# Performance work log

Measured on AMD Instinct MI355X. Metric: run time of the kernel, lower is better.

The kernel has to match this reference:

```python
import jax, jax.numpy as jnp
import numpy as np

N_NODES = 100000
N_EDGES = 3200000
D_IN = 128
D_HID = 128
N_CLASSES = 40


def setup_inputs() -> dict:
    key = jax.random.key(0)
    ks = jax.random.split(key, 8)
    x = jax.random.normal(ks[0], (N_NODES, D_IN), dtype=jnp.float32)
    edge_index = jax.random.randint(ks[1], (2, N_EDGES), 0, N_NODES, dtype=jnp.int64)
    s1 = 1.0 / np.sqrt(D_IN)
    s2 = 1.0 / np.sqrt(D_HID)
    W1 = jax.random.normal(ks[2], (D_IN, D_HID), dtype=jnp.float32) * s1
    b1 = jnp.zeros((D_HID,), dtype=jnp.float32)
    W2 = jax.random.normal(ks[3], (D_HID, D_HID), dtype=jnp.float32) * s2
    b2 = jnp.zeros((D_HID,), dtype=jnp.float32)
    Wl = jax.random.normal(ks[4], (D_HID, N_CLASSES), dtype=jnp.float32) * s2
    bl = jnp.zeros((N_CLASSES,), dtype=jnp.float32)
    return {"x": x, "edge_index": edge_index, "W1": W1, "b1": b1,
            "W2": W2, "b2": b2, "Wl": Wl, "bl": bl}


def _gcn_conv(x, W, b, src, dst, inv_sqrt_deg, n_nodes):
    # h = X @ W  (linear transform first: cheaper when out_dim <= in_dim)
    h = x @ W  # [N, d_out]
    # symmetric normalization: norm_e = deg(src)^-1/2 * deg(dst)^-1/2
    norm = inv_sqrt_deg[src] * inv_sqrt_deg[dst]  # [E]
    msg = h[src] * norm[:, None]                  # gather + scale  [E, d_out]
    out = jax.ops.segment_sum(msg, dst, num_segments=n_nodes)  # scatter-add
    return out + b


def reference(x, edge_index, W1, b1, W2, b2, Wl, bl):
    n = x.shape[0]
    # GCNConv adds self-loops before normalization (PyG default)
    loops = jnp.arange(n, dtype=edge_index.dtype)
    src = jnp.concatenate([edge_index[0], loops])
    dst = jnp.concatenate([edge_index[1], loops])
    deg = jax.ops.segment_sum(jnp.ones_like(dst, dtype=x.dtype), dst, num_segments=n)
    inv_sqrt_deg = jnp.where(deg > 0, jax.lax.rsqrt(deg), 0.0)

    h = _gcn_conv(x, W1, b1, src, dst, inv_sqrt_deg, n)
    h = jax.nn.relu(h)
    h = _gcn_conv(h, W2, b2, src, dst, inv_sqrt_deg, n)
    h = jax.nn.relu(h)
    return h @ Wl + bl
```

## Files before the change

kernel.cpp:

```cpp
#include <hip/hip_runtime.h>
#include <hip/hip_bf16.h>

typedef _Float16 f16;
typedef _Float16 f16x8 __attribute__((ext_vector_type(8)));

#define D 128
#define N_CLS 40
#define BN 128
#define NBMAX 1024


__global__ __launch_bounds__(256) void k_hist(const int* __restrict__ dst,
                                              int* __restrict__ bcnt, int e) {
  __shared__ int lh[NBMAX];
  for (int j = threadIdx.x; j < NBMAX; j += 256) lh[j] = 0;
  __syncthreads();
  int stride = gridDim.x * blockDim.x;
  for (int q = blockIdx.x * blockDim.x + threadIdx.x; q < e; q += stride)
    atomicAdd(&lh[dst[q] >> 7], 1);
  __syncthreads();
  for (int j = threadIdx.x; j < NBMAX; j += 256)
    if (lh[j]) atomicAdd(&bcnt[j], lh[j]);
}

__global__ __launch_bounds__(1024) void k_bscan(const int* __restrict__ bcnt,
                                                int* __restrict__ bbase,
                                                int* __restrict__ bcur) {
  __shared__ int sums[NBMAX];
  int t = threadIdx.x;
  int c = bcnt[t];
  sums[t] = c;
  __syncthreads();
  for (int off = 1; off < NBMAX; off <<= 1) {
    int a = (t >= off) ? sums[t - off] : 0;
    __syncthreads();
    sums[t] += a;
    __syncthreads();
  }
  bbase[t] = sums[t] - c;
  bcur[t] = sums[t] - c;
}

__global__ __launch_bounds__(256) void k_place(const int* __restrict__ src,
                                               const int* __restrict__ dst,
                                               int* __restrict__ bcur,
                                               unsigned int* __restrict__ binned,
                                               int e, int nwg) {
  __shared__ int lh[NBMAX];
  __shared__ int lofs[NBMAX];
  __shared__ int lcur[NBMAX];
  int chunk = (e + nwg - 1) / nwg;
  int lo = blockIdx.x * chunk;
  int hi = min(e, lo + chunk);
  int t = threadIdx.x;
  for (int j = t; j < NBMAX; j += 256) { lh[j] = 0; lcur[j] = 0; }
  __syncthreads();
  for (int q = lo + t; q < hi; q += 256) atomicAdd(&lh[dst[q] >> 7], 1);
  __syncthreads();
  for (int j = t; j < NBMAX; j += 256) {
    int c = lh[j];
    lofs[j] = c ? atomicAdd(&bcur[j], c) : 0;
  }
  __syncthreads();
  for (int q = lo + t; q < hi; q += 256) {
    int d = dst[q];
    int b = d >> 7;
    int r = atomicAdd(&lcur[b], 1);
    binned[lofs[b] + r] = ((unsigned int)(d & 127) << 17) | (unsigned int)src[q];
  }
}

__global__ __launch_bounds__(256) void k_csr(const unsigned int* __restrict__ binned,
                                             const int* __restrict__ bbase,
                                             int* __restrict__ csr,
                                             int* __restrict__ deg,
                                             float* __restrict__ isd,
                                             int* __restrict__ row_start, int n) {
  int b = blockIdx.x;
  int lo = bbase[b], hi = bbase[b + 1];
  __shared__ int h[BN];
  __shared__ int sc[BN];
  __shared__ int cur[BN];
  int t = threadIdx.x;
  if (t < BN) h[t] = 0;
  __syncthreads();
  for (int q = lo + t; q < hi; q += 256) atomicAdd(&h[binned[q] >> 17], 1);
  __syncthreads();
  if (t < BN) sc[t] = h[t];
  __syncthreads();
  for (int off = 1; off < BN; off <<= 1) {
    int a = 0;
    if (t < BN && t >= off) a = sc[t - off];
    __syncthreads();
    if (t < BN) sc[t] += a;
    __syncthreads();
  }
  if (t < BN) {
    int excl = sc[t] - h[t];
    cur[t] = lo + excl;
    int i = b * BN + t;
    if (i < n) {
      deg[i] = h[t];
      isd[i] = rsqrtf((float)(h[t] + 1));
      row_start[i] = lo + excl;
    }
  }
  __syncthreads();
  for (int q = lo + t; q < hi; q += 256) {
    unsigned int u = binned[q];
    int p = atomicAdd(&cur[u >> 17], 1);
    csr[p] = (int)(u & 0x1FFFF);
  }
}

template <bool HALF_IN>
__global__ __launch_bounds__(256) void k_gemm_t(const void* __restrict__ Xv,
                                                const float* __restrict__ W,
                                                const float* __restrict__ isd,
                                                f16* __restrict__ HS, int n) {
  __shared__ float Xt[64][D + 4];
  __shared__ float Wb[32][D + 4];
  const size_t ss = (size_t)n * 16;
  int t = threadIdx.x;
  int r0 = blockIdx.x * 64;
  if (!HALF_IN) {
    const float* X = (const float*)Xv;
    for (int q = t; q < 64 * 32; q += 256) {
      int row = q >> 5, cb = (q & 31) << 2;
      float4 v = {0.f, 0.f, 0.f, 0.f};
      if (r0 + row < n) v = *(const float4*)(X + (size_t)(r0 + row) * D + cb);
      *(float4*)&Xt[row][cb] = v;
    }
  } else {
    const f16* X = (const f16*)Xv;
    for (int q = t; q < 64 * 16; q += 256) {
      int row = q >> 4, cb = (q & 15) << 3;
      f16x8 v = 0;
      if (r0 + row < n)
        v = *(const f16x8*)(X + (size_t)(cb >> 4) * ss +
                            (size_t)(r0 + row) * 16 + (cb & 15));
      float* xp = &Xt[row][cb];
#pragma unroll
      for (int j = 0; j < 8; ++j) xp[j] = (float)v[j];
    }
  }
  int tr = ((t >> 4) & 15) << 2;
  int tc = (t & 15) << 3;
  float acc[4][8];
#pragma unroll
  for (int i = 0; i < 4; ++i)
#pragma unroll
    for (int j = 0; j < 8; ++j) acc[i][j] = 0.f;

  for (int hh = 0; hh < 4; ++hh) {
    __syncthreads();
    for (int q = t; q < 32 * 32; q += 256) {
      int row = q >> 5, cb = (q & 31) << 2;
      *(float4*)&Wb[row][cb] = *(const float4*)(W + (size_t)(hh * 32 + row) * D + cb);
    }
    __syncthreads();
#pragma unroll 4
    for (int k = 0; k < 32; ++k) {
      float4 u0 = *(const float4*)&Wb[k][tc];
      float4 u1 = *(const float4*)&Wb[k][tc + 4];
      float bv[8] = {u0.x, u0.y, u0.z, u0.w, u1.x, u1.y, u1.z, u1.w};
      int kk = hh * 32 + k;
#pragma unroll
      for (int i = 0; i < 4; ++i) {
        float a = Xt[tr + i][kk];
#pragma unroll
        for (int j = 0; j < 8; ++j) acc[i][j] += a * bv[j];
      }
    }
  }
#pragma unroll
  for (int i = 0; i < 4; ++i) {
    int row = r0 + tr + i;
    if (row < n) {
      float s = isd[row];
      f16x8 ov;
#pragma unroll
      for (int j = 0; j < 8; ++j) ov[j] = (f16)(s * acc[i][j]);
      *(f16x8*)(HS + (size_t)(tc >> 4) * ss + (size_t)row * 16 + (tc & 15)) = ov;
    }
  }
}

__device__ inline f16x8 shfl_xor_f16x8(f16x8 v, int m) {
  union { f16x8 h; int i[4]; } u;
  u.h = v;
#pragma unroll
  for (int k = 0; k < 4; ++k) u.i[k] = __shfl_xor(u.i[k], m);
  return u.h;
}

__global__ __launch_bounds__(256) void k_aggs(const f16* __restrict__ HS,
                                              const int* __restrict__ csr,
                                              const int* __restrict__ row_start,
                                              const int* __restrict__ deg,
                                              const float* __restrict__ isd,
                                              const float* __restrict__ bias,
                                              f16* __restrict__ G, int n) {
  const size_t ss = (size_t)n * 16;
  int t = threadIdx.x;
  int wave = t >> 6, lane = t & 63;
  int g = lane >> 4, r = lane & 15;
  int s = blockIdx.x & 7;
  int i0 = ((blockIdx.x >> 3) << 4) + (wave << 2) + g;
  bool ok = i0 < n;
  int i = ok ? i0 : n - 1;
  int hf = r & 1, er = r >> 1;
  int dg = deg[i];
  const int* cp = csr + row_start[i];
  const f16* sb = HS + (size_t)s * ss + (size_t)hf * 8;
  f16x8 a0 = (f16x8)0, a1 = (f16x8)0;
  if (dg > 0) {
    int dgm = dg - 1;
    int iA = cp[min(er, dgm)];
    int iB = cp[min(er + 8, dgm)];
    for (int u = 0; u < dg; u += 16) {
      int cA = iA, cB = iB;
      iA = cp[min(u + 16 + er, dgm)];
      iB = cp[min(u + 24 + er, dgm)];
      if (u + er < dg)
        a0 += *(const f16x8*)(sb + ((size_t)(unsigned)cA << 4));
      if (u + 8 + er < dg)
        a1 += *(const f16x8*)(sb + ((size_t)(unsigned)cB << 4));
    }
  }
  f16x8 tv = a0 + a1;
  tv += shfl_xor_f16x8(tv, 2);
  tv += shfl_xor_f16x8(tv, 4);
  tv += shfl_xor_f16x8(tv, 8);
  f16x8 sv = *(const f16x8*)(HS + (size_t)s * ss + (size_t)i * 16 + hf * 8);
  float di = isd[i];
  const float* bp = bias + s * 16 + hf * 8;
  float4 b0 = *(const float4*)bp;
  float4 b1 = *(const float4*)(bp + 4);
  float bv[8] = {b0.x, b0.y, b0.z, b0.w, b1.x, b1.y, b1.z, b1.w};
  f16x8 ov;
#pragma unroll
  for (int j = 0; j < 8; ++j) {
    float v = di * ((float)tv[j] + (float)sv[j]) + bv[j];
    v = v > 0.f ? v : 0.f;
    ov[j] = (f16)v;
  }
  if (ok && r < 2)
    *(f16x8*)(G + (size_t)s * ss + (size_t)i * 16 + hf * 8) = ov;
}

__global__ __launch_bounds__(256) void k_cls(const f16* __restrict__ H,
                                             const float* __restrict__ Wl,
                                             const float* __restrict__ bl,
                                             float* __restrict__ out, int n) {
  const size_t ss = (size_t)n * 16;
  int wv = threadIdx.x >> 6;
  int ir = (blockIdx.x << 2) + wv;
  int i = ir < n ? ir : n - 1;
  int lane = threadIdx.x & 63;
  __shared__ float tt[4][D];
  if (lane < 16) {
    int s = lane >> 1, hf = lane & 1;
    f16x8 v = *(const f16x8*)(H + (size_t)s * ss + (size_t)i * 16 + hf * 8);
    float* dp = &tt[wv][s * 16 + hf * 8];
#pragma unroll
    for (int j = 0; j < 8; ++j) dp[j] = (float)v[j];
  }
  __syncthreads();
  if (ir < n && lane < N_CLS) {
    float o = bl[lane];
#pragma unroll 4
    for (int k = 0; k < D; k += 4) {
      float4 t4 = *(const float4*)&tt[wv][k];
      o += t4.x * Wl[(k + 0) * N_CLS + lane];
      o += t4.y * Wl[(k + 1) * N_CLS + lane];
      o += t4.z * Wl[(k + 2) * N_CLS + lane];
      o += t4.w * Wl[(k + 3) * N_CLS + lane];
    }
    out[(size_t)ir * N_CLS + lane] = o;
  }
}

extern "C" void kernel_launch(void* const* d_in, const int* in_sizes, int n_in,
                              void* d_out, int out_size, void* d_ws, size_t ws_size,
                              hipStream_t stream) {
  const float* x  = (const float*)d_in[0];
  const int*   ei = (const int*)d_in[1];
  const float* W1 = (const float*)d_in[2];
  const float* b1 = (const float*)d_in[3];
  const float* W2 = (const float*)d_in[4];
  const float* b2 = (const float*)d_in[5];
  const float* Wl = (const float*)d_in[6];
  const float* bl = (const float*)d_in[7];
  float* out = (float*)d_out;

  const int n = in_sizes[0] / D;
  const int e = in_sizes[1] / 2;
  const int* src = ei;
  const int* dst = ei + e;
  const int nb = (n + BN - 1) / BN;

  char* ws = (char*)d_ws;
  size_t off = 0;
  auto alloc = [&](size_t bytes) -> void* {
    void* p = ws + off;
    off += (bytes + 255) & ~(size_t)255;
    return p;
  };
  int*   bcnt      = (int*)alloc(NBMAX * 4);
  int*   bbase     = (int*)alloc(NBMAX * 4);
  int*   bcur      = (int*)alloc(NBMAX * 4);
  int*   deg       = (int*)alloc((size_t)n * 4);
  int*   row_start = (int*)alloc((size_t)n * 4);
  float* isd       = (float*)alloc((size_t)n * 4);
  int*   csr       = (int*)alloc((size_t)e * 4);
  f16*   hA        = (f16*)alloc((size_t)n * D * 2);
  f16*   hB        = (f16*)alloc((size_t)n * D * 2);
  unsigned int* binned = (unsigned int*)hA;

  hipMemsetAsync(bcnt, 0, NBMAX * 4, stream);

  const int nwg_place = 512;
  k_hist<<<1024, 256, 0, stream>>>(dst, bcnt, e);
  k_bscan<<<1, 1024, 0, stream>>>(bcnt, bbase, bcur);
  k_place<<<nwg_place, 256, 0, stream>>>(src, dst, bcur, binned, e, nwg_place);
  k_csr<<<nb, 256, 0, stream>>>(binned, bbase, csr, deg, isd, row_start, n);

  int gblocks = (n + 63) / 64;
  int ablocks = ((n + 15) / 16) * 8;
  k_gemm_t<false><<<gblocks, 256, 0, stream>>>(x, W1, isd, hA, n);
  k_aggs<<<ablocks, 256, 0, stream>>>(hA, csr, row_start, deg, isd, b1, hB, n);
  k_gemm_t<true><<<gblocks, 256, 0, stream>>>(hB, W2, isd, hA, n);
  k_aggs<<<ablocks, 256, 0, stream>>>(hA, csr, row_start, deg, isd, b2, hB, n);
  k_cls<<<(n + 3) / 4, 256, 0, stream>>>(hB, Wl, bl, out, n);
}
```

Before: 679.9 us.

## Use row-major aggregation output, widen edge unroll, batch classifier rows per block

The aggregation kernel now writes its output row-major ([n, 128] f16) instead of in 16-column slabs. The half-precision GEMM input path and the classifier read that layout with contiguous row loads. The edge loop keeps four accumulators and prefetches 32 neighbor indices per iteration instead of 16, to expose more memory-level parallelism on the gathers. The classifier stages 16 rows per block in shared memory, with each wave computing 4 rows. The padded D+1 row stride makes the float4 shared-memory reads misaligned for odd rows, which risks slower LDS access or incorrect behaviour.

```diff
diff --git a/kernel.cpp b/kernel.cpp
--- a/kernel.cpp
+++ b/kernel.cpp
@@ -136,9 +136,7 @@
     for (int q = t; q < 64 * 16; q += 256) {
       int row = q >> 4, cb = (q & 15) << 3;
       f16x8 v = 0;
-      if (r0 + row < n)
-        v = *(const f16x8*)(X + (size_t)(cb >> 4) * ss +
-                            (size_t)(r0 + row) * 16 + (cb & 15));
+      if (r0 + row < n) v = *(const f16x8*)(X + (size_t)(r0 + row) * D + cb);
       float* xp = &Xt[row][cb];
 #pragma unroll
       for (int j = 0; j < 8; ++j) xp[j] = (float)v[j];
@@ -212,29 +210,37 @@
   int hf = r & 1, er = r >> 1;
   int dg = deg[i];
   const int* cp = csr + row_start[i];
-  const f16* sb = HS + (size_t)s * ss + (size_t)hf * 8;
-  f16x8 a0 = (f16x8)0, a1 = (f16x8)0;
+  const f16* sb = HS + (size_t)s * ss + (size_t)(hf << 3);
+  f16x8 a0 = (f16x8)0, a1 = (f16x8)0, a2 = (f16x8)0, a3 = (f16x8)0;
   if (dg > 0) {
     int dgm = dg - 1;
     int iA = cp[min(er, dgm)];
     int iB = cp[min(er + 8, dgm)];
-    for (int u = 0; u < dg; u += 16) {
-      int cA = iA, cB = iB;
-      iA = cp[min(u + 16 + er, dgm)];
-      iB = cp[min(u + 24 + er, dgm)];
+    int iC = cp[min(er + 16, dgm)];
+    int iD = cp[min(er + 24, dgm)];
+    for (int u = 0; u < dg; u += 32) {
+      int cA = iA, cB = iB, cC = iC, cD = iD;
+      iA = cp[min(u + 32 + er, dgm)];
+      iB = cp[min(u + 40 + er, dgm)];
+      iC = cp[min(u + 48 + er, dgm)];
+      iD = cp[min(u + 56 + er, dgm)];
       if (u + er < dg)
         a0 += *(const f16x8*)(sb + ((size_t)(unsigned)cA << 4));
       if (u + 8 + er < dg)
         a1 += *(const f16x8*)(sb + ((size_t)(unsigned)cB << 4));
-    }
-  }
-  f16x8 tv = a0 + a1;
+      if (u + 16 + er < dg)
+        a2 += *(const f16x8*)(sb + ((size_t)(unsigned)cC << 4));
+      if (u + 24 + er < dg)
+        a3 += *(const f16x8*)(sb + ((size_t)(unsigned)cD << 4));
+    }
+  }
+  f16x8 tv = (a0 + a1) + (a2 + a3);
   tv += shfl_xor_f16x8(tv, 2);
   tv += shfl_xor_f16x8(tv, 4);
   tv += shfl_xor_f16x8(tv, 8);
-  f16x8 sv = *(const f16x8*)(HS + (size_t)s * ss + (size_t)i * 16 + hf * 8);
+  f16x8 sv = *(const f16x8*)(HS + (size_t)s * ss + (size_t)i * 16 + (hf << 3));
   float di = isd[i];
-  const float* bp = bias + s * 16 + hf * 8;
+  const float* bp = bias + s * 16 + (hf << 3);
   float4 b0 = *(const float4*)bp;
   float4 b1 = *(const float4*)(bp + 4);
   float bv[8] = {b0.x, b0.y, b0.z, b0.w, b1.x, b1.y, b1.z, b1.w};
@@ -246,38 +252,43 @@
     ov[j] = (f16)v;
   }
   if (ok && r < 2)
-    *(f16x8*)(G + (size_t)s * ss + (size_t)i * 16 + hf * 8) = ov;
+    *(f16x8*)(G + (size_t)i * D + s * 16 + (hf << 3)) = ov;
 }
 
 __global__ __launch_bounds__(256) void k_cls(const f16* __restrict__ H,
                                              const float* __restrict__ Wl,
                                              const float* __restrict__ bl,
                                              float* __restrict__ out, int n) {
-  const size_t ss = (size_t)n * 16;
-  int wv = threadIdx.x >> 6;
-  int ir = (blockIdx.x << 2) + wv;
-  int i = ir < n ? ir : n - 1;
-  int lane = threadIdx.x & 63;
-  __shared__ float tt[4][D];
-  if (lane < 16) {
-    int s = lane >> 1, hf = lane & 1;
-    f16x8 v = *(const f16x8*)(H + (size_t)s * ss + (size_t)i * 16 + hf * 8);
-    float* dp = &tt[wv][s * 16 + hf * 8];
+  __shared__ float tt[16][D + 1];
+  int t = threadIdx.x;
+  int i0 = blockIdx.x << 4;
+  {
+    int row = t >> 4, part = t & 15;
+    int ir = i0 + row;
+    f16x8 v = (f16x8)0;
+    if (ir < n) v = *(const f16x8*)(H + (size_t)ir * D + part * 8);
+    float* dp = &tt[row][part * 8];
 #pragma unroll
     for (int j = 0; j < 8; ++j) dp[j] = (float)v[j];
   }
   __syncthreads();
-  if (ir < n && lane < N_CLS) {
-    float o = bl[lane];
+  int wv = t >> 6, lane = t & 63;
+  if (lane < N_CLS) {
+    for (int nd = 0; nd < 4; ++nd) {
+      int ir = i0 + wv * 4 + nd;
+      if (ir >= n) break;
+      const float* tp = tt[wv * 4 + nd];
+      float o = bl[lane];
 #pragma unroll 4
-    for (int k = 0; k < D; k += 4) {
-      float4 t4 = *(const float4*)&tt[wv][k];
-      o += t4.x * Wl[(k + 0) * N_CLS + lane];
-      o += t4.y * Wl[(k + 1) * N_CLS + lane];
-      o += t4.z * Wl[(k + 2) * N_CLS + lane];
-      o += t4.w * Wl[(k + 3) * N_CLS + lane];
-    }
-    out[(size_t)ir * N_CLS + lane] = o;
+      for (int k = 0; k < D; k += 4) {
+        float4 t4 = *(const float4*)&tp[k];
+        o += t4.x * Wl[(k + 0) * N_CLS + lane];
+        o += t4.y * Wl[(k + 1) * N_CLS + lane];
+        o += t4.z * Wl[(k + 2) * N_CLS + lane];
+        o += t4.w * Wl[(k + 3) * N_CLS + lane];
+      }
+      out[(size_t)ir * N_CLS + lane] = o;
+    }
   }
 }
 
@@ -332,5 +343,5 @@
   k_aggs<<<ablocks, 256, 0, stream>>>(hA, csr, row_start, deg, isd, b1, hB, n);
   k_gemm_t<true><<<gblocks, 256, 0, stream>>>(hB, W2, isd, hA, n);
   k_aggs<<<ablocks, 256, 0, stream>>>(hA, csr, row_start, deg, isd, b2, hB, n);
-  k_cls<<<(n + 3) / 4, 256, 0, stream>>>(hB, Wl, bl, out, n);
-}
+  k_cls<<<(n + 15) / 16, 256, 0, stream>>>(hB, Wl, bl, out, n);
+}
```

Measured after the change: 766.4 us. 1.13x slower.
